# Optimization experiments

Measured on AMD Instinct MI355X. Metric: run time of the kernel, lower is better.

## Reference

```python
import jax, jax.numpy as jnp
import numpy as np


def setup_inputs() -> dict:
    key = jax.random.key(0)
    kx, kr, kq, kk, kv = jax.random.split(key, 5)
    B, T, N, C = 4, 8, 2048, 128
    w_scale = 1.0 / np.sqrt(C)  # keep logits in a sane range
    return {
        "x": jax.random.normal(kx, (B, T, N, C), dtype=jnp.float32),
        "residual_source": jax.random.normal(kr, (B, N, C), dtype=jnp.float32),
        "Wq": jax.random.normal(kq, (C, C), dtype=jnp.float32) * w_scale,
        "Wk": jax.random.normal(kk, (C, C), dtype=jnp.float32) * w_scale,
        "Wv": jax.random.normal(kv, (C, C), dtype=jnp.float32) * w_scale,
    }


def reference(x, residual_source, Wq, Wk, Wv):
    # x: [B, T, N, C]; residual_source: [B, M, C] (expanded along T in the
    # original via unsqueeze+expand; here we exploit broadcasting instead of
    # materializing the [B, T, M, C] copy -- same math, k/v identical per T).
    q = jnp.einsum("btnc,cd->btnd", x, Wq)               # [B, T, N, D]
    k = jnp.einsum("bmc,cd->bmd", residual_source, Wk)   # [B, M, D]
    v = jnp.einsum("bmc,cd->bmd", residual_source, Wv)   # [B, M, D]
    # Unscaled attention, exactly as in the original (no 1/sqrt(d)).
    affinities = jnp.einsum("btnd,bmd->btnm", q, k)       # [B, T, N, M]
    attn = jax.nn.softmax(affinities, axis=-1)
    residual = jnp.einsum("btnm,bmd->btnd", attn, v)      # [B, T, N, D]
    return x + residual
```

## Files before the change

### kernel.cpp

```cpp
#include <hip/hip_runtime.h>


#define Bn 4
#define Tn 8
#define Nn 2048
#define Cn 128
#define Mn 2048
#define NTILES 32
#define QROWS 128
#define NQT (Nn / QROWS)

typedef __attribute__((ext_vector_type(4))) float f32x4;
typedef __attribute__((ext_vector_type(8))) _Float16 f16x8;
typedef __attribute__((address_space(3))) unsigned char lds_uc;
typedef const __attribute__((address_space(1))) unsigned char glb_uc;

__device__ __forceinline__ unsigned short f2h(float f) {
  _Float16 h = (_Float16)f;
  return __builtin_bit_cast(unsigned short, h);
}
__device__ __forceinline__ unsigned int pk2(float a, float b) {
  auto v = __builtin_amdgcn_cvt_pkrtz(a, b);
  return __builtin_bit_cast(unsigned int, v);
}
__device__ __forceinline__ f16x8 lds_read8w(const unsigned char* base, int row,
                                            int colByte) {
  int byte = row * 256 + (colByte ^ ((row & 15) << 4));
  return *(const f16x8*)(base + byte);
}
__device__ __forceinline__ void gld16(const void* g, void* l) {
  __builtin_amdgcn_global_load_lds((glb_uc*)g, (lds_uc*)l, 16, 0, 0);
}

__global__ __launch_bounds__(256) void proj_kv_kernel(
    const float* __restrict__ rs, const float* __restrict__ Wk,
    const float* __restrict__ Wv, unsigned short* __restrict__ k_ws,
    unsigned short* __restrict__ vt_ws) {
  __shared__ unsigned char smem[48 * 1024];
  unsigned char* rsh = smem;
  unsigned char* wt = smem + 16 * 1024;

  const int bid = blockIdx.x;
  const int b = bid >> 5;
  const int kt = bid & 31;
  const int m0 = kt << 6;
  const int tid = threadIdx.x;
  const int wv = tid >> 6, lane = tid & 63;

  {
    const float4* g = (const float4*)(rs + ((size_t)b * Mn + m0) * Cn);
#pragma unroll
    for (int i = 0; i < 8; ++i) {
      int f = tid + i * 256;
      int row = f >> 5, c4 = f & 31;
      float4 v = g[f];
      int byte = row * 256 + ((c4 * 8) ^ ((row & 15) << 4));
      *(ushort4*)(rsh + byte) =
          make_ushort4(f2h(v.x), f2h(v.y), f2h(v.z), f2h(v.w));
    }
  }

#define STAGE_WT(Wp)                                                          \
  {                                                                           \
    const float4* g = (const float4*)(Wp);                                    \
    _Pragma("unroll") for (int i = 0; i < 16; ++i) {                          \
      int f = tid + i * 256;                                                  \
      int cc = f >> 5, d0 = (f & 31) * 4;                                     \
      float4 v = g[f];                                                        \
      float vv[4] = {v.x, v.y, v.z, v.w};                                     \
      _Pragma("unroll") for (int j = 0; j < 4; ++j) {                         \
        int row = d0 + j;                                                     \
        int byte = row * 256 + ((cc * 2) ^ ((row & 15) << 4));                \
        *(unsigned short*)(wt + byte) = f2h(vv[j]);                           \
      }                                                                       \
    }                                                                         \
  }

  STAGE_WT(Wk);
  __syncthreads();

  const int arow = wv * 16 + (lane & 15);
  f16x8 ah[4];
#pragma unroll
  for (int ks = 0; ks < 4; ++ks)
    ah[ks] = lds_read8w(rsh, arow, (lane >> 4) * 16 + ks * 64);

  f32x4 acc[8];
#pragma unroll
  for (int df = 0; df < 8; ++df) acc[df] = (f32x4)(0.0f);
#pragma unroll
  for (int ks = 0; ks < 4; ++ks)
#pragma unroll
    for (int df = 0; df < 8; ++df) {
      f16x8 bf = lds_read8w(wt, df * 16 + (lane & 15), (lane >> 4) * 16 + ks * 64);
      acc[df] = __builtin_amdgcn_mfma_f32_16x16x32_f16(ah[ks], bf, acc[df], 0, 0, 0);
    }
  {
    unsigned char* kb = (unsigned char*)k_ws + ((size_t)b * NTILES + kt) * 16384;
#pragma unroll
    for (int df = 0; df < 8; ++df)
#pragma unroll
      for (int r = 0; r < 4; ++r) {
        int row = wv * 16 + (lane >> 4) * 4 + r;
        int dcol = df * 16 + (lane & 15);
        int byte = row * 256 + ((dcol * 2) ^ ((row & 15) << 4));
        *(unsigned short*)(kb + byte) = f2h(acc[df][r]);
      }
  }
  __syncthreads();

  STAGE_WT(Wv);
  __syncthreads();
#pragma unroll
  for (int df = 0; df < 8; ++df) acc[df] = (f32x4)(0.0f);
#pragma unroll
  for (int ks = 0; ks < 4; ++ks)
#pragma unroll
    for (int df = 0; df < 8; ++df) {
      f16x8 bf = lds_read8w(wt, df * 16 + (lane & 15), (lane >> 4) * 16 + ks * 64);
      acc[df] = __builtin_amdgcn_mfma_f32_16x16x32_f16(ah[ks], bf, acc[df], 0, 0, 0);
    }
  {
    unsigned char* vb = (unsigned char*)vt_ws + ((size_t)b * NTILES + kt) * 16384;
#pragma unroll
    for (int df = 0; df < 8; ++df)
#pragma unroll
      for (int r = 0; r < 4; ++r) {
        int row = wv * 16 + (lane >> 4) * 4 + r;
        int dcol = df * 16 + (lane & 15);
        int srow = dcol >> 1;
        int byte = srow * 256 +
                   ((((dcol & 1) << 7) | (row * 2)) ^ ((srow & 15) << 4));
        *(unsigned short*)(vb + byte) = f2h(acc[df][r]);
      }
  }
#undef STAGE_WT
}

__global__ __launch_bounds__(256, 2) void attn_kernel(
    const float* __restrict__ x, const float* __restrict__ Wq,
    const unsigned short* __restrict__ k_ws,
    const unsigned short* __restrict__ vt_ws, float* __restrict__ out) {
  __shared__ unsigned char smem[80 * 1024];

  const int bx = blockIdx.x;
  const int wb = ((bx & 7) << 6) | (bx >> 3);
  const int b = wb >> 7;
  const int t_ = (wb >> 4) & 7;
  const int n0 = (wb & 15) * QROWS;
  const int tid = threadIdx.x;
  const int wv = tid >> 6, lane = tid & 63;
  const int c = lane & 15, g = lane >> 4;

  const float* xg = x + (((size_t)b * Tn + t_) * Nn + n0) * Cn;
  unsigned char* xa = smem;
  unsigned char* wqb = smem + 32 * 1024;
  unsigned char* pb = smem + 64 * 1024 + wv * 4096;

  const float LOG2E = 1.4426950408889634f;
  {
    const float4* gp = (const float4*)xg;
#pragma unroll
    for (int ii = 0; ii < 16; ++ii) {
      int f = tid + ii * 256;
      int row = f >> 5, c4 = f & 31;
      float4 v = gp[f];
      int byte = row * 256 + ((c4 * 8) ^ ((row & 15) << 4));
      *(ushort4*)(xa + byte) =
          make_ushort4(f2h(v.x), f2h(v.y), f2h(v.z), f2h(v.w));
    }
  }
  {
    const float4* gp = (const float4*)Wq;
#pragma unroll
    for (int ii = 0; ii < 16; ++ii) {
      int f = tid + ii * 256;
      int cc = f >> 5, d0 = (f & 31) * 4;
      float4 v = gp[f];
      float vv[4] = {v.x, v.y, v.z, v.w};
#pragma unroll
      for (int j = 0; j < 4; ++j) {
        int row = d0 + j;
        int byte = row * 256 + ((cc * 2) ^ ((row & 15) << 4));
        *(unsigned short*)(wqb + byte) = f2h(vv[j] * LOG2E);
      }
    }
  }
  __syncthreads();

  f32x4 qacc[2][8];
#pragma unroll
  for (int rb = 0; rb < 2; ++rb)
#pragma unroll
    for (int df = 0; df < 8; ++df) qacc[rb][df] = (f32x4)(0.0f);
  {
    f16x8 xf[2][4];
#pragma unroll
    for (int rb = 0; rb < 2; ++rb)
#pragma unroll
      for (int ks = 0; ks < 4; ++ks)
        xf[rb][ks] = lds_read8w(xa, wv * 32 + rb * 16 + c, g * 16 + ks * 64);
#pragma unroll
    for (int ks = 0; ks < 4; ++ks)
#pragma unroll
      for (int df = 0; df < 8; ++df) {
        f16x8 bf = lds_read8w(wqb, df * 16 + c, g * 16 + ks * 64);
        qacc[0][df] = __builtin_amdgcn_mfma_f32_16x16x32_f16(xf[0][ks], bf, qacc[0][df], 0, 0, 0);
        qacc[1][df] = __builtin_amdgcn_mfma_f32_16x16x32_f16(xf[1][ks], bf, qacc[1][df], 0, 0, 0);
      }
  }
#pragma unroll
  for (int rb = 0; rb < 2; ++rb)
#pragma unroll
    for (int df = 0; df < 8; ++df)
#pragma unroll
      for (int r = 0; r < 4; ++r) {
        int row = wv * 32 + rb * 16 + g * 4 + r;
        int col = df * 16 + c;
        int byte = row * 256 + ((col * 2) ^ ((row & 15) << 4));
        *(unsigned short*)(xa + byte) = f2h(qacc[rb][df][r]);
      }
  f16x8 qf[2][4];
#pragma unroll
  for (int rb = 0; rb < 2; ++rb)
#pragma unroll
    for (int ks = 0; ks < 4; ++ks)
      qf[rb][ks] = lds_read8w(xa, wv * 32 + rb * 16 + c, g * 16 + ks * 64);
  __syncthreads();

  f32x4 o[2][8];
#pragma unroll
  for (int rb = 0; rb < 2; ++rb)
#pragma unroll
    for (int df = 0; df < 8; ++df) o[rb][df] = (f32x4)(0.0f);
  float mrow[2] = {-INFINITY, -INFINITY};
  float lrow[2] = {0.f, 0.f};

  const unsigned char* khg = (const unsigned char*)k_ws + (size_t)b * NTILES * 16384;
  const unsigned char* vtg = (const unsigned char*)vt_ws + (size_t)b * NTILES * 16384;

  auto stage = [&](unsigned char* buf, int kt) {
    const unsigned char* kh = khg + (size_t)kt * 16384;
    const unsigned char* vt = vtg + (size_t)kt * 16384;
    int o16 = tid * 16;
#pragma unroll
    for (int h = 0; h < 4; ++h) {
      gld16(kh + o16 + h * 4096, buf + o16 + h * 4096);
      gld16(vt + o16 + h * 4096, buf + 16384 + o16 + h * 4096);
    }
  };

  auto do_tile = [&](unsigned char* buf) {
    unsigned char* kh = buf;
    unsigned char* vt = buf + 16384;
    f32x4 st[2][4];
#pragma unroll
    for (int rb = 0; rb < 2; ++rb)
#pragma unroll
      for (int kvb = 0; kvb < 4; ++kvb) st[rb][kvb] = (f32x4)(0.0f);
    __builtin_amdgcn_s_setprio(1);
#pragma unroll
    for (int ks = 0; ks < 4; ++ks)
#pragma unroll
      for (int kvb = 0; kvb < 4; ++kvb) {
        f16x8 kf = lds_read8w(kh, kvb * 16 + c, g * 16 + ks * 64);
        st[0][kvb] = __builtin_amdgcn_mfma_f32_16x16x32_f16(kf, qf[0][ks], st[0][kvb], 0, 0, 0);
        st[1][kvb] = __builtin_amdgcn_mfma_f32_16x16x32_f16(kf, qf[1][ks], st[1][kvb], 0, 0, 0);
      }
    __builtin_amdgcn_s_setprio(0);

#pragma unroll
    for (int rb = 0; rb < 2; ++rb) {
      float tm = st[rb][0][0];
#pragma unroll
      for (int kvb = 0; kvb < 4; ++kvb)
#pragma unroll
        for (int r = 0; r < 4; ++r) tm = fmaxf(tm, st[rb][kvb][r]);
      if (__any(tm > mrow[rb] + 8.f)) {
        tm = fmaxf(tm, __shfl_xor(tm, 16));
        tm = fmaxf(tm, __shfl_xor(tm, 32));
        float newm = fmaxf(mrow[rb], tm);
        float scl = exp2f(mrow[rb] - newm);
#pragma unroll
        for (int df = 0; df < 8; ++df) o[rb][df] *= scl;
        lrow[rb] *= scl;
        mrow[rb] = newm;
      }
      float mn = mrow[rb];
      float ps = 0.f;
      int swz = (c & 15) << 4;
#pragma unroll
      for (int kvb = 0; kvb < 4; ++kvb) {
        float p0 = exp2f(st[rb][kvb][0] - mn);
        float p1 = exp2f(st[rb][kvb][1] - mn);
        float p2 = exp2f(st[rb][kvb][2] - mn);
        float p3 = exp2f(st[rb][kvb][3] - mn);
        ps += (p0 + p1) + (p2 + p3);
        int kv2 = rb * 128 + kvb * 32 + g * 8;
        *(unsigned int*)(pb + c * 256 + (kv2 ^ swz)) = pk2(p0, p1);
        *(unsigned int*)(pb + c * 256 + ((kv2 + 4) ^ swz)) = pk2(p2, p3);
      }
      lrow[rb] += ps;
    }

    f16x8 pa[2][2];
#pragma unroll
    for (int rb = 0; rb < 2; ++rb)
#pragma unroll
      for (int ks = 0; ks < 2; ++ks)
        pa[rb][ks] = lds_read8w(pb, c, rb * 128 + g * 16 + ks * 64);

    __builtin_amdgcn_s_setprio(1);
#pragma unroll
    for (int ks = 0; ks < 2; ++ks)
#pragma unroll
      for (int df = 0; df < 8; ++df) {
        int d = df * 16 + c;
        int srow = d >> 1;
        int byte = srow * 256 +
                   ((((d & 1) << 7) | (g * 16 + ks * 64)) ^ ((srow & 15) << 4));
        f16x8 vf = *(const f16x8*)(vt + byte);
        o[0][df] = __builtin_amdgcn_mfma_f32_16x16x32_f16(vf, pa[0][ks], o[0][df], 0, 0, 0);
        o[1][df] = __builtin_amdgcn_mfma_f32_16x16x32_f16(vf, pa[1][ks], o[1][df], 0, 0, 0);
      }
    __builtin_amdgcn_s_setprio(0);
  };

  unsigned char* B0 = smem;
  unsigned char* B1 = smem + 32 * 1024;
  stage(B0, 0);
  __syncthreads();
#pragma unroll 1
  for (int it = 0; it < 16; ++it) {
    int kt = it * 2;
    stage(B1, kt + 1);
    do_tile(B0);
    __syncthreads();
    if (kt + 2 < NTILES) stage(B0, kt + 2);
    do_tile(B1);
    __syncthreads();
  }

#pragma unroll
  for (int rb = 0; rb < 2; ++rb) {
    lrow[rb] += __shfl_xor(lrow[rb], 16);
    lrow[rb] += __shfl_xor(lrow[rb], 32);
  }
  float inv[2] = {1.0f / lrow[0], 1.0f / lrow[1]};
#pragma unroll
  for (int rb = 0; rb < 2; ++rb)
#pragma unroll
    for (int df = 0; df < 8; ++df)
#pragma unroll
      for (int r = 0; r < 4; ++r) {
        int row = wv * 32 + rb * 16 + c;
        int d = df * 16 + g * 4 + r;
        int byte = row * 512 + ((d * 4) ^ ((row & 7) << 4));
        *(float*)(smem + byte) = o[rb][df][r] * inv[rb];
      }
  __syncthreads();
  {
    const float4* xg4 = (const float4*)xg;
    float4* og4 = (float4*)(out + (((size_t)b * Tn + t_) * Nn + n0) * Cn);
#pragma unroll
    for (int ii = 0; ii < 16; ++ii) {
      int f = tid + ii * 256;
      int row = f >> 5, c4 = f & 31;
      int byte = row * 512 + ((c4 * 16) ^ ((row & 7) << 4));
      f32x4 v = *(const f32x4*)(smem + byte);
      float4 xv = xg4[f];
      og4[f] = make_float4(xv.x + v[0], xv.y + v[1], xv.z + v[2], xv.w + v[3]);
    }
  }
}

extern "C" void kernel_launch(void* const* d_in, const int* in_sizes, int n_in,
                              void* d_out, int out_size, void* d_ws,
                              size_t ws_size, hipStream_t stream) {
  const float* x = (const float*)d_in[0];
  const float* rs = (const float*)d_in[1];
  const float* Wq = (const float*)d_in[2];
  const float* Wk = (const float*)d_in[3];
  const float* Wv = (const float*)d_in[4];
  float* out = (float*)d_out;

  unsigned short* k_ws = (unsigned short*)d_ws;
  unsigned short* vt_ws = k_ws + (size_t)Bn * Mn * Cn;

  proj_kv_kernel<<<Bn * NTILES, 256, 0, stream>>>(rs, Wk, Wv, k_ws, vt_ws);
  attn_kernel<<<Bn * Tn * NQT, 256, 0, stream>>>(x, Wq, k_ws, vt_ws, out);
}
```

Baseline: 127.3 us.

## Switch attention to 32x32x16 MFMA with register-resident P via permlane swap

Rewrites the attention inner loop to use 32x32x16 f16 MFMAs on 64-key tiles, so each wave handles 32 query rows as one block. The P matrix is repacked in registers with v_permlane32_swap instead of being written to and read back from a per-wave LDS buffer. The V tile is stored in a 128-byte-row layout to match. This removes the LDS round trip for P and the extra cross-lane reductions, and cuts LDS to 64KB. It also changes the pipeline to one tile per loop iteration with a single barrier, which needs careful checking of the V layout and permlane semantics for correctness.

```diff
diff --git a/kernel.cpp b/kernel.cpp
--- a/kernel.cpp
+++ b/kernel.cpp
@@ -11,7 +11,9 @@
 #define NQT (Nn / QROWS)
 
 typedef __attribute__((ext_vector_type(4))) float f32x4;
+typedef __attribute__((ext_vector_type(16))) float f32x16;
 typedef __attribute__((ext_vector_type(8))) _Float16 f16x8;
+typedef __attribute__((ext_vector_type(4))) unsigned int u32x4;
 typedef __attribute__((address_space(3))) unsigned char lds_uc;
 typedef const __attribute__((address_space(1))) unsigned char glb_uc;
 
@@ -28,9 +30,26 @@
   int byte = row * 256 + (colByte ^ ((row & 15) << 4));
   return *(const f16x8*)(base + byte);
 }
+__device__ __forceinline__ f16x8 lds_read8v(const unsigned char* base, int row,
+                                            int colByte) {
+  int byte = row * 128 + (colByte ^ ((row & 7) << 4));
+  return *(const f16x8*)(base + byte);
+}
 __device__ __forceinline__ void gld16(const void* g, void* l) {
   __builtin_amdgcn_global_load_lds((glb_uc*)g, (lds_uc*)l, 16, 0, 0);
 }
+
+#define MKPF(dst, sv, base)                                        \
+  {                                                                \
+    unsigned a0 = pk2(sv[base + 0], sv[base + 1]);                 \
+    unsigned b0 = pk2(sv[base + 4], sv[base + 5]);                 \
+    unsigned a1 = pk2(sv[base + 2], sv[base + 3]);                 \
+    unsigned b1 = pk2(sv[base + 6], sv[base + 7]);                 \
+    asm("v_permlane32_swap_b32 %0, %1" : "+v"(a0), "+v"(b0));      \
+    asm("v_permlane32_swap_b32 %0, %1" : "+v"(a1), "+v"(b1));      \
+    u32x4 tmp = {a0, a1, b0, b1};                                  \
+    dst = __builtin_bit_cast(f16x8, tmp);                          \
+  }
 
 __global__ __launch_bounds__(256) void proj_kv_kernel(
     const float* __restrict__ rs, const float* __restrict__ Wk,
@@ -128,9 +147,7 @@
       for (int r = 0; r < 4; ++r) {
         int row = wv * 16 + (lane >> 4) * 4 + r;
         int dcol = df * 16 + (lane & 15);
-        int srow = dcol >> 1;
-        int byte = srow * 256 +
-                   ((((dcol & 1) << 7) | (row * 2)) ^ ((srow & 15) << 4));
+        int byte = dcol * 128 + ((row * 2) ^ ((dcol & 7) << 4));
         *(unsigned short*)(vb + byte) = f2h(acc[df][r]);
       }
   }
@@ -141,7 +158,7 @@
     const float* __restrict__ x, const float* __restrict__ Wq,
     const unsigned short* __restrict__ k_ws,
     const unsigned short* __restrict__ vt_ws, float* __restrict__ out) {
-  __shared__ unsigned char smem[80 * 1024];
+  __shared__ unsigned char smem[64 * 1024];
 
   const int bx = blockIdx.x;
   const int wb = ((bx & 7) << 6) | (bx >> 3);
@@ -151,11 +168,11 @@
   const int tid = threadIdx.x;
   const int wv = tid >> 6, lane = tid & 63;
   const int c = lane & 15, g = lane >> 4;
+  const int l31 = lane & 31, hi = lane >> 5;
 
   const float* xg = x + (((size_t)b * Tn + t_) * Nn + n0) * Cn;
   unsigned char* xa = smem;
   unsigned char* wqb = smem + 32 * 1024;
-  unsigned char* pb = smem + 64 * 1024 + wv * 4096;
 
   const float LOG2E = 1.4426950408889634f;
   {
@@ -188,12 +205,12 @@
   }
   __syncthreads();
 
-  f32x4 qacc[2][8];
-#pragma unroll
-  for (int rb = 0; rb < 2; ++rb)
-#pragma unroll
-    for (int df = 0; df < 8; ++df) qacc[rb][df] = (f32x4)(0.0f);
-  {
+  {
+    f32x4 qacc[2][8];
+#pragma unroll
+    for (int rb = 0; rb < 2; ++rb)
+#pragma unroll
+      for (int df = 0; df < 8; ++df) qacc[rb][df] = (f32x4)(0.0f);
     f16x8 xf[2][4];
 #pragma unroll
     for (int rb = 0; rb < 2; ++rb)
@@ -208,156 +225,140 @@
         qacc[0][df] = __builtin_amdgcn_mfma_f32_16x16x32_f16(xf[0][ks], bf, qacc[0][df], 0, 0, 0);
         qacc[1][df] = __builtin_amdgcn_mfma_f32_16x16x32_f16(xf[1][ks], bf, qacc[1][df], 0, 0, 0);
       }
-  }
-#pragma unroll
-  for (int rb = 0; rb < 2; ++rb)
-#pragma unroll
-    for (int df = 0; df < 8; ++df)
-#pragma unroll
-      for (int r = 0; r < 4; ++r) {
-        int row = wv * 32 + rb * 16 + g * 4 + r;
-        int col = df * 16 + c;
-        int byte = row * 256 + ((col * 2) ^ ((row & 15) << 4));
-        *(unsigned short*)(xa + byte) = f2h(qacc[rb][df][r]);
-      }
-  f16x8 qf[2][4];
-#pragma unroll
-  for (int rb = 0; rb < 2; ++rb)
-#pragma unroll
-    for (int ks = 0; ks < 4; ++ks)
-      qf[rb][ks] = lds_read8w(xa, wv * 32 + rb * 16 + c, g * 16 + ks * 64);
-  __syncthreads();
-
-  f32x4 o[2][8];
-#pragma unroll
-  for (int rb = 0; rb < 2; ++rb)
-#pragma unroll
-    for (int df = 0; df < 8; ++df) o[rb][df] = (f32x4)(0.0f);
-  float mrow[2] = {-INFINITY, -INFINITY};
-  float lrow[2] = {0.f, 0.f};
+#pragma unroll
+    for (int rb = 0; rb < 2; ++rb)
+#pragma unroll
+      for (int df = 0; df < 8; ++df)
+#pragma unroll
+        for (int r = 0; r < 4; ++r) {
+          int row = wv * 32 + rb * 16 + g * 4 + r;
+          int col = df * 16 + c;
+          int byte = row * 256 + ((col * 2) ^ ((row & 15) << 4));
+          *(unsigned short*)(xa + byte) = f2h(qacc[rb][df][r]);
+        }
+  }
+  f16x8 qf[8];
+#pragma unroll
+  for (int kc = 0; kc < 8; ++kc)
+    qf[kc] = lds_read8w(xa, wv * 32 + l31, kc * 32 + hi * 16);
+  __syncthreads();
+
+  f32x16 o[4];
+#pragma unroll
+  for (int dblk = 0; dblk < 4; ++dblk) o[dblk] = (f32x16)(0.0f);
+  float mrow = -INFINITY;
+  float lrow = 0.f;
 
   const unsigned char* khg = (const unsigned char*)k_ws + (size_t)b * NTILES * 16384;
   const unsigned char* vtg = (const unsigned char*)vt_ws + (size_t)b * NTILES * 16384;
 
-  auto stage = [&](unsigned char* buf, int kt) {
-    const unsigned char* kh = khg + (size_t)kt * 16384;
-    const unsigned char* vt = vtg + (size_t)kt * 16384;
-    int o16 = tid * 16;
+  auto stage = [&](int t) {
+    unsigned char* kd = smem + (t & 1) * 16384 + tid * 16;
+    unsigned char* vd = smem + 32 * 1024 + (t & 1) * 16384 + tid * 16;
+    const unsigned char* ksrc = khg + (size_t)t * 16384 + tid * 16;
+    const unsigned char* vsrc = vtg + (size_t)t * 16384 + tid * 16;
 #pragma unroll
     for (int h = 0; h < 4; ++h) {
-      gld16(kh + o16 + h * 4096, buf + o16 + h * 4096);
-      gld16(vt + o16 + h * 4096, buf + 16384 + o16 + h * 4096);
+      gld16(ksrc + h * 4096, kd + h * 4096);
+      gld16(vsrc + h * 4096, vd + h * 4096);
     }
   };
 
-  auto do_tile = [&](unsigned char* buf) {
-    unsigned char* kh = buf;
-    unsigned char* vt = buf + 16384;
-    f32x4 st[2][4];
-#pragma unroll
-    for (int rb = 0; rb < 2; ++rb)
-#pragma unroll
-      for (int kvb = 0; kvb < 4; ++kvb) st[rb][kvb] = (f32x4)(0.0f);
+  stage(0);
+  __syncthreads();
+
+#pragma unroll 1
+  for (int t = 0; t < NTILES; ++t) {
+    unsigned char* kb = smem + (t & 1) * 16384;
+    unsigned char* vb = smem + 32 * 1024 + (t & 1) * 16384;
+    if (t + 1 < NTILES) stage(t + 1);
+
+    f32x16 s0 = (f32x16)(0.0f), s1 = (f32x16)(0.0f);
     __builtin_amdgcn_s_setprio(1);
 #pragma unroll
-    for (int ks = 0; ks < 4; ++ks)
-#pragma unroll
-      for (int kvb = 0; kvb < 4; ++kvb) {
-        f16x8 kf = lds_read8w(kh, kvb * 16 + c, g * 16 + ks * 64);
-        st[0][kvb] = __builtin_amdgcn_mfma_f32_16x16x32_f16(kf, qf[0][ks], st[0][kvb], 0, 0, 0);
-        st[1][kvb] = __builtin_amdgcn_mfma_f32_16x16x32_f16(kf, qf[1][ks], st[1][kvb], 0, 0, 0);
-      }
+    for (int kc = 0; kc < 8; ++kc) {
+      f16x8 kf0 = lds_read8w(kb, l31, kc * 32 + hi * 16);
+      f16x8 kf1 = lds_read8w(kb, 32 + l31, kc * 32 + hi * 16);
+      s0 = __builtin_amdgcn_mfma_f32_32x32x16_f16(kf0, qf[kc], s0, 0, 0, 0);
+      s1 = __builtin_amdgcn_mfma_f32_32x32x16_f16(kf1, qf[kc], s1, 0, 0, 0);
+    }
     __builtin_amdgcn_s_setprio(0);
 
-#pragma unroll
-    for (int rb = 0; rb < 2; ++rb) {
-      float tm = st[rb][0][0];
-#pragma unroll
-      for (int kvb = 0; kvb < 4; ++kvb)
-#pragma unroll
-        for (int r = 0; r < 4; ++r) tm = fmaxf(tm, st[rb][kvb][r]);
-      if (__any(tm > mrow[rb] + 8.f)) {
-        tm = fmaxf(tm, __shfl_xor(tm, 16));
-        tm = fmaxf(tm, __shfl_xor(tm, 32));
-        float newm = fmaxf(mrow[rb], tm);
-        float scl = exp2f(mrow[rb] - newm);
-#pragma unroll
-        for (int df = 0; df < 8; ++df) o[rb][df] *= scl;
-        lrow[rb] *= scl;
-        mrow[rb] = newm;
-      }
-      float mn = mrow[rb];
+    float tm;
+    {
+      float mx[16];
+#pragma unroll
+      for (int r = 0; r < 16; ++r) mx[r] = fmaxf(s0[r], s1[r]);
+#pragma unroll
+      for (int r = 0; r < 8; ++r) mx[r] = fmaxf(mx[r], mx[r + 8]);
+#pragma unroll
+      for (int r = 0; r < 4; ++r) mx[r] = fmaxf(mx[r], mx[r + 4]);
+      tm = fmaxf(fmaxf(mx[0], mx[1]), fmaxf(mx[2], mx[3]));
+    }
+    tm = fmaxf(tm, __shfl_xor(tm, 32));
+    if (__any(tm > mrow + 8.f)) {
+      float newm = fmaxf(mrow, tm);
+      float scl = exp2f(mrow - newm);
+#pragma unroll
+      for (int dblk = 0; dblk < 4; ++dblk) o[dblk] *= scl;
+      lrow *= scl;
+      mrow = newm;
+    }
+    {
       float ps = 0.f;
-      int swz = (c & 15) << 4;
-#pragma unroll
-      for (int kvb = 0; kvb < 4; ++kvb) {
-        float p0 = exp2f(st[rb][kvb][0] - mn);
-        float p1 = exp2f(st[rb][kvb][1] - mn);
-        float p2 = exp2f(st[rb][kvb][2] - mn);
-        float p3 = exp2f(st[rb][kvb][3] - mn);
-        ps += (p0 + p1) + (p2 + p3);
-        int kv2 = rb * 128 + kvb * 32 + g * 8;
-        *(unsigned int*)(pb + c * 256 + (kv2 ^ swz)) = pk2(p0, p1);
-        *(unsigned int*)(pb + c * 256 + ((kv2 + 4) ^ swz)) = pk2(p2, p3);
-      }
-      lrow[rb] += ps;
-    }
-
-    f16x8 pa[2][2];
-#pragma unroll
-    for (int rb = 0; rb < 2; ++rb)
-#pragma unroll
-      for (int ks = 0; ks < 2; ++ks)
-        pa[rb][ks] = lds_read8w(pb, c, rb * 128 + g * 16 + ks * 64);
+#pragma unroll
+      for (int r = 0; r < 16; ++r) {
+        float p = exp2f(s0[r] - mrow);
+        s0[r] = p;
+        ps += p;
+      }
+#pragma unroll
+      for (int r = 0; r < 16; ++r) {
+        float p = exp2f(s1[r] - mrow);
+        s1[r] = p;
+        ps += p;
+      }
+      lrow += ps;
+    }
+
+    f16x8 pf0, pf1, pf2, pf3;
+    MKPF(pf0, s0, 0);
+    MKPF(pf1, s0, 8);
+    MKPF(pf2, s1, 0);
+    MKPF(pf3, s1, 8);
 
     __builtin_amdgcn_s_setprio(1);
 #pragma unroll
-    for (int ks = 0; ks < 2; ++ks)
-#pragma unroll
-      for (int df = 0; df < 8; ++df) {
-        int d = df * 16 + c;
-        int srow = d >> 1;
-        int byte = srow * 256 +
-                   ((((d & 1) << 7) | (g * 16 + ks * 64)) ^ ((srow & 15) << 4));
-        f16x8 vf = *(const f16x8*)(vt + byte);
-        o[0][df] = __builtin_amdgcn_mfma_f32_16x16x32_f16(vf, pa[0][ks], o[0][df], 0, 0, 0);
-        o[1][df] = __builtin_amdgcn_mfma_f32_16x16x32_f16(vf, pa[1][ks], o[1][df], 0, 0, 0);
-      }
+    for (int dblk = 0; dblk < 4; ++dblk) {
+      f16x8 vf0 = lds_read8v(vb, dblk * 32 + l31, 0 * 32 + hi * 16);
+      f16x8 vf1 = lds_read8v(vb, dblk * 32 + l31, 1 * 32 + hi * 16);
+      f16x8 vf2 = lds_read8v(vb, dblk * 32 + l31, 2 * 32 + hi * 16);
+      f16x8 vf3 = lds_read8v(vb, dblk * 32 + l31, 3 * 32 + hi * 16);
+      o[dblk] = __builtin_amdgcn_mfma_f32_32x32x16_f16(vf0, pf0, o[dblk], 0, 0, 0);
+      o[dblk] = __builtin_amdgcn_mfma_f32_32x32x16_f16(vf1, pf1, o[dblk], 0, 0, 0);
+      o[dblk] = __builtin_amdgcn_mfma_f32_32x32x16_f16(vf2, pf2, o[dblk], 0, 0, 0);
+      o[dblk] = __builtin_amdgcn_mfma_f32_32x32x16_f16(vf3, pf3, o[dblk], 0, 0, 0);
+    }
     __builtin_amdgcn_s_setprio(0);
-  };
-
-  unsigned char* B0 = smem;
-  unsigned char* B1 = smem + 32 * 1024;
-  stage(B0, 0);
-  __syncthreads();
-#pragma unroll 1
-  for (int it = 0; it < 16; ++it) {
-    int kt = it * 2;
-    stage(B1, kt + 1);
-    do_tile(B0);
     __syncthreads();
-    if (kt + 2 < NTILES) stage(B0, kt + 2);
-    do_tile(B1);
-    __syncthreads();
-  }
-
-#pragma unroll
-  for (int rb = 0; rb < 2; ++rb) {
-    lrow[rb] += __shfl_xor(lrow[rb], 16);
-    lrow[rb] += __shfl_xor(lrow[rb], 32);
-  }
-  float inv[2] = {1.0f / lrow[0], 1.0f / lrow[1]};
-#pragma unroll
-  for (int rb = 0; rb < 2; ++rb)
-#pragma unroll
-    for (int df = 0; df < 8; ++df)
-#pragma unroll
-      for (int r = 0; r < 4; ++r) {
-        int row = wv * 32 + rb * 16 + c;
-        int d = df * 16 + g * 4 + r;
-        int byte = row * 512 + ((d * 4) ^ ((row & 7) << 4));
-        *(float*)(smem + byte) = o[rb][df][r] * inv[rb];
-      }
+  }
+
+  lrow += __shfl_xor(lrow, 32);
+  float inv = 1.0f / lrow;
+#pragma unroll
+  for (int dblk = 0; dblk < 4; ++dblk)
+#pragma unroll
+    for (int rg = 0; rg < 4; ++rg) {
+      f32x4 v;
+      v[0] = o[dblk][rg * 4 + 0] * inv;
+      v[1] = o[dblk][rg * 4 + 1] * inv;
+      v[2] = o[dblk][rg * 4 + 2] * inv;
+      v[3] = o[dblk][rg * 4 + 3] * inv;
+      int row = wv * 32 + l31;
+      int colb = dblk * 128 + rg * 32 + hi * 16;
+      int byte = row * 512 + (colb ^ ((row & 7) << 4));
+      *(f32x4*)(smem + byte) = v;
+    }
   __syncthreads();
   {
     const float4* xg4 = (const float4*)xg;
@@ -365,8 +366,8 @@
 #pragma unroll
     for (int ii = 0; ii < 16; ++ii) {
       int f = tid + ii * 256;
-      int row = f >> 5, c4 = f & 31;
-      int byte = row * 512 + ((c4 * 16) ^ ((row & 7) << 4));
+      int row = f >> 5, slot = f & 31;
+      int byte = row * 512 + ((slot * 16) ^ ((row & 7) << 4));
       f32x4 v = *(const f32x4*)(smem + byte);
       float4 xv = xg4[f];
       og4[f] = make_float4(xv.x + v[0], xv.y + v[1], xv.z + v[2], xv.w + v[3]);
```

New measurement: 121.8 us, median of 2. 4.3% less time.
